# Kernel optimization log

Measured on AMD Instinct MI355X. Metric: run time of the kernel, lower is better.

Reference implementation:

```python
import jax, jax.numpy as jnp
import numpy as np

N_HEAD = 16


def setup_inputs() -> dict:
    key = jax.random.key(0)
    ks = jax.random.split(key, 9)
    B, T, C = 4, 2048, 1024
    s = 1.0 / np.sqrt(C)
    x = jax.random.normal(ks[0], (B, T, C), dtype=jnp.float32)
    Wq = jax.random.normal(ks[1], (C, C), dtype=jnp.float32) * s
    bq = jnp.zeros((C,), dtype=jnp.float32)
    Wk = jax.random.normal(ks[2], (C, C), dtype=jnp.float32) * s
    bk = jnp.zeros((C,), dtype=jnp.float32)
    Wv = jax.random.normal(ks[3], (C, C), dtype=jnp.float32) * s
    bv = jnp.zeros((C,), dtype=jnp.float32)
    Wp = jax.random.normal(ks[4], (C, C), dtype=jnp.float32) * s
    bp = jnp.zeros((C,), dtype=jnp.float32)
    return {"x": x, "Wq": Wq, "bq": bq, "Wk": Wk, "bk": bk,
            "Wv": Wv, "bv": bv, "Wp": Wp, "bp": bp}


def reference(x, Wq, bq, Wk, bk, Wv, bv, Wp, bp):
    B, T, C = x.shape
    H = N_HEAD
    D = C // H
    # QKV projections, then split heads: [B, T, C] -> [B, H, T, D]
    def split_heads(t):
        return t.reshape(B, T, H, D).transpose(0, 2, 1, 3)
    q = split_heads(x @ Wq.T + bq)
    k = split_heads(x @ Wk.T + bk)
    v = split_heads(x @ Wv.T + bv)
    # NOTE: original code applies NO causal mask despite the class name.
    att = jnp.einsum('bhtd,bhsd->bhts', q, k) * (1.0 / jnp.sqrt(jnp.float32(D)))
    att = jax.nn.softmax(att, axis=-1)
    y = jnp.einsum('bhts,bhsd->bhtd', att, v)  # [B, H, T, D]
    y = y.transpose(0, 2, 1, 3).reshape(B, T, C)
    return y @ Wp.T + bp
```

## Files before the change

### kernel.cpp

```cpp
#include <hip/hip_runtime.h>
#include <hip/hip_bf16.h>

typedef float  f32x4   __attribute__((ext_vector_type(4)));
typedef short  bf16x8  __attribute__((ext_vector_type(8)));

__device__ __forceinline__ ushort f2b(float f) {
  union { float f; unsigned u; } x; x.f = f;
  unsigned r = x.u + 0x7fffu + ((x.u >> 16) & 1u);
  return (ushort)(r >> 16);
}

__device__ __forceinline__ unsigned pk2(float lo, float hi) {
  __hip_bfloat162 t = __float22bfloat162_rn(make_float2(lo, hi));
  union { __hip_bfloat162 b; unsigned u; } c; c.b = t; return c.u;
}

__device__ __forceinline__ f32x4 fzero() {
  f32x4 z; z[0] = 0.f; z[1] = 0.f; z[2] = 0.f; z[3] = 0.f; return z;
}

__device__ __forceinline__ void gld_lds16(const ushort* g, ushort* l) {
  __builtin_amdgcn_global_load_lds(g, l, 16, 0, 0);
}

__device__ __forceinline__ int vperm_s(int j64) {
  return (j64 & 0x23) | ((j64 & 0x0C) << 1) | ((j64 & 0x10) >> 2);
}

__global__ __launch_bounds__(256) void f2bf_kernel(const float* __restrict__ in,
                                                   ushort* __restrict__ out, int n4) {
  int idx = blockIdx.x * 256 + threadIdx.x;
  int stride = gridDim.x * 256;
  for (int i = idx; i < n4; i += stride) {
    float4 v = reinterpret_cast<const float4*>(in)[i];
    ushort4 o;
    o.x = f2b(v.x); o.y = f2b(v.y); o.z = f2b(v.z); o.w = f2b(v.w);
    reinterpret_cast<ushort4*>(out)[i] = o;
  }
}

__global__ __launch_bounds__(256) void f2bf_w4(
    const float* __restrict__ w0, const float* __restrict__ w1,
    const float* __restrict__ w2, const float* __restrict__ w3,
    ushort* __restrict__ out, int n4) {
  const float* src = (blockIdx.y == 0) ? w0 : (blockIdx.y == 1) ? w1
                   : (blockIdx.y == 2) ? w2 : w3;
  ushort* dst = out + (size_t)blockIdx.y * (size_t)n4 * 4;
  int idx = blockIdx.x * 256 + threadIdx.x;
  int stride = gridDim.x * 256;
  for (int i = idx; i < n4; i += stride) {
    float4 v = reinterpret_cast<const float4*>(src)[i];
    ushort4 o;
    o.x = f2b(v.x); o.y = f2b(v.y); o.z = f2b(v.z); o.w = f2b(v.w);
    reinterpret_cast<ushort4*>(dst)[i] = o;
  }
}

__global__ __launch_bounds__(256) void gemm_bt_n64(
    const ushort* __restrict__ A, const ushort* __restrict__ B,
    const float* __restrict__ bias, float* __restrict__ Cf,
    int M, int N, int K) {
  __shared__ ushort As[128 * 32];
  __shared__ ushort Bs[64 * 32];
  const int tid = threadIdx.x, lane = tid & 63, wave = tid >> 6;
  const int wr = (wave >> 1) << 6, wc = (wave & 1) << 5;
  const int fr = lane & 15, fk8 = (lane >> 4) << 3;

  const size_t rowA = (size_t)blockIdx.y * 128;
  const size_t rowB = (size_t)blockIdx.x * 64;
  const ushort* Ag = A + rowA * K;
  const ushort* Bg = B + rowB * K;

  const int c0 = tid, c1 = tid + 256;
  const size_t a0 = (size_t)(c0 >> 2) * K + (size_t)((c0 & 3) << 3);
  const size_t a1 = (size_t)(c1 >> 2) * K + (size_t)((c1 & 3) << 3);

  f32x4 acc[4][2];
#pragma unroll
  for (int m = 0; m < 4; ++m)
#pragma unroll
    for (int n = 0; n < 2; ++n) acc[m][n] = fzero();

  for (int k0 = 0; k0 < K; k0 += 32) {
    __syncthreads();
    gld_lds16(Ag + a0 + k0, &As[wave * 512]);
    gld_lds16(Ag + a1 + k0, &As[2048 + wave * 512]);
    gld_lds16(Bg + a0 + k0, &Bs[wave * 512]);
    asm volatile("s_waitcnt vmcnt(0)" ::: "memory");
    __syncthreads();

    bf16x8 af[4], bfv[2];
#pragma unroll
    for (int m = 0; m < 4; ++m)
      af[m] = *reinterpret_cast<const bf16x8*>(&As[(wr + m * 16 + fr) * 32 + fk8]);
#pragma unroll
    for (int n = 0; n < 2; ++n)
      bfv[n] = *reinterpret_cast<const bf16x8*>(&Bs[(wc + n * 16 + fr) * 32 + fk8]);
#pragma unroll
    for (int m = 0; m < 4; ++m)
#pragma unroll
      for (int n = 0; n < 2; ++n)
        acc[m][n] = __builtin_amdgcn_mfma_f32_16x16x32_bf16(af[m], bfv[n], acc[m][n], 0, 0, 0);
  }

  const int orow = (lane >> 4) << 2;
#pragma unroll
  for (int m = 0; m < 4; ++m) {
#pragma unroll
    for (int n = 0; n < 2; ++n) {
      size_t gc = rowB + wc + n * 16 + fr;
      float bv = bias[gc];
#pragma unroll
      for (int r = 0; r < 4; ++r) {
        size_t gr = rowA + wr + m * 16 + orow + r;
        Cf[gr * N + gc] = acc[m][n][r] + bv;
      }
    }
  }
}

__global__ __launch_bounds__(256) void gemm_qkv(
    const ushort* __restrict__ A, const ushort* __restrict__ Bw,
    const float* __restrict__ bq, const float* __restrict__ bk, const float* __restrict__ bv,
    ushort* __restrict__ Qb, ushort* __restrict__ Kb, ushort* __restrict__ VbT,
    float qscale) {
  __shared__ ushort As[128 * 32];
  __shared__ ushort Bs[128 * 32];
  const int tid = threadIdx.x, lane = tid & 63, wave = tid >> 6;
  const int wr = (wave >> 1) << 6, wc = (wave & 1) << 6;
  const int fr = lane & 15, fk8 = (lane >> 4) << 3;
  const int K = 1024;

  const size_t rowA = (size_t)blockIdx.y * 128;
  const size_t rowB = (size_t)blockIdx.x * 128;
  const ushort* Ag = A + rowA * K;
  const ushort* Bg = Bw + rowB * K;

  const int c0 = tid, c1 = tid + 256;
  const size_t a0 = (size_t)(c0 >> 2) * K + (size_t)((c0 & 3) << 3);
  const size_t a1 = (size_t)(c1 >> 2) * K + (size_t)((c1 & 3) << 3);

  f32x4 acc[4][4];
#pragma unroll
  for (int m = 0; m < 4; ++m)
#pragma unroll
    for (int n = 0; n < 4; ++n) acc[m][n] = fzero();

  for (int k0 = 0; k0 < K; k0 += 32) {
    __syncthreads();
    gld_lds16(Ag + a0 + k0, &As[wave * 512]);
    gld_lds16(Ag + a1 + k0, &As[2048 + wave * 512]);
    gld_lds16(Bg + a0 + k0, &Bs[wave * 512]);
    gld_lds16(Bg + a1 + k0, &Bs[2048 + wave * 512]);
    asm volatile("s_waitcnt vmcnt(0)" ::: "memory");
    __syncthreads();

    bf16x8 af[4], bfv[4];
#pragma unroll
    for (int m = 0; m < 4; ++m)
      af[m] = *reinterpret_cast<const bf16x8*>(&As[(wr + m * 16 + fr) * 32 + fk8]);
#pragma unroll
    for (int n = 0; n < 4; ++n)
      bfv[n] = *reinterpret_cast<const bf16x8*>(&Bs[(wc + n * 16 + fr) * 32 + fk8]);
#pragma unroll
    for (int m = 0; m < 4; ++m)
#pragma unroll
      for (int n = 0; n < 4; ++n)
        acc[m][n] = __builtin_amdgcn_mfma_f32_16x16x32_bf16(af[m], bfv[n], acc[m][n], 0, 0, 0);
  }

  const int stripe  = blockIdx.x >> 3;
  const int colbase = (blockIdx.x & 7) * 128;
  const int orow = (lane >> 4) << 2;
#pragma unroll
  for (int m = 0; m < 4; ++m) {
#pragma unroll
    for (int n = 0; n < 4; ++n) {
      const int gcl = colbase + wc + n * 16 + fr;
      if (stripe == 0) {
        const float bb_ = bq[gcl];
#pragma unroll
        for (int r = 0; r < 4; ++r) {
          size_t gr = rowA + wr + m * 16 + orow + r;
          Qb[gr * 1024 + gcl] = f2b((acc[m][n][r] + bb_) * qscale);
        }
      } else if (stripe == 1) {
        const float bb_ = bk[gcl];
#pragma unroll
        for (int r = 0; r < 4; ++r) {
          size_t gr = rowA + wr + m * 16 + orow + r;
          Kb[gr * 1024 + gcl] = f2b(acc[m][n][r] + bb_);
        }
      } else {
        const float bb_ = bv[gcl];
        int tt0 = (int)rowA + wr + m * 16 + orow;
        int b = tt0 >> 11, t = tt0 & 2047;
        size_t idx0 = (size_t)b * 2097152 + (size_t)gcl * 2048
                    + (size_t)((t & ~63) + vperm_s(t & 63));
        ushort4 o;
        o.x = f2b(acc[m][n][0] + bb_);
        o.y = f2b(acc[m][n][1] + bb_);
        o.z = f2b(acc[m][n][2] + bb_);
        o.w = f2b(acc[m][n][3] + bb_);
        *reinterpret_cast<ushort4*>(&VbT[idx0]) = o;
      }
    }
  }
}

__global__ __launch_bounds__(512, 4) void attn_kernel(
    const ushort* __restrict__ Qb, const ushort* __restrict__ Kb,
    const ushort* __restrict__ VbT, ushort* __restrict__ Yb) {
  __shared__ ushort lds[16384];
  const int tid = threadIdx.x, lane = tid & 63, wave = tid >> 6;
  const int fr = lane & 15, g = lane >> 4, fk8 = g << 3;
  const int bb = blockIdx.y >> 4, hh = blockIdx.y & 15;
  const size_t rowbase = (size_t)bb * 2048;
  const int cbase = hh * 64;
  const ushort* Kg  = Kb  + rowbase * 1024 + cbase;
  const ushort* VgT = VbT + (size_t)bb * 2097152 + (size_t)cbase * 2048;

  const int qrow = blockIdx.x * 128 + wave * 16 + fr;
  const ushort* qptr = &Qb[(rowbase + qrow) * 1024 + cbase];
  const bf16x8 qf0 = *reinterpret_cast<const bf16x8*>(qptr + fk8);
  const bf16x8 qf1 = *reinterpret_cast<const bf16x8*>(qptr + 32 + fk8);

  const int rS = tid >> 3;
  const int wS = (tid & 7) ^ (rS & 7);
  const ushort* sKp = Kg  + (size_t)rS * 1024 + (wS << 3);
  const ushort* sVp = VgT + (size_t)rS * 2048 + (wS << 3);
  const int wofs = wave * 512;

  const int e0 = (g ^ (fr & 7)) << 3;
  const int e1 = ((4 + g) ^ (fr & 7)) << 3;
  const ushort* lpA = &lds[fr * 64 + e0];
  const ushort* lpB = &lds[fr * 64 + e1];

  f32x4 yacc[4];
#pragma unroll
  for (int nb = 0; nb < 4; ++nb) yacc[nb] = fzero();
  f32x4 psum4 = fzero();

#define LD8(P) (*reinterpret_cast<const bf16x8*>(P))
#define MF16(A, B, C) __builtin_amdgcn_mfma_f32_16x16x32_bf16(A, B, C, 0, 0, 0)

  gld_lds16(sKp, &lds[wofs]);  gld_lds16(sVp, &lds[8192 + wofs]);  sKp += 65536; sVp += 64;
  asm volatile("s_waitcnt vmcnt(0)" ::: "memory");
  __builtin_amdgcn_s_barrier();
  __builtin_amdgcn_sched_barrier(0);

#define TILE(BUF, DOPF) do {                                                     \
    if (DOPF) {    \
      gld_lds16(sKp, &lds[((BUF) ^ 1) * 4096 + wofs]);                           \
      gld_lds16(sVp, &lds[8192 + ((BUF) ^ 1) * 4096 + wofs]);                    \
      sKp += 65536; sVp += 64;                                                   \
    }                                                                            \
    f32x4 sT[4];                                                                 \
    _Pragma("unroll")                                                            \
    for (int jb = 0; jb < 4; ++jb) {                                             \
      bf16x8 kf0 = LD8(lpA + (BUF) * 4096 + jb * 1024);                          \
      bf16x8 kf1 = LD8(lpB + (BUF) * 4096 + jb * 1024);                          \
      f32x4 z = fzero();                                                         \
      __builtin_amdgcn_s_setprio(1);                                             \
      z = MF16(kf0, qf0, z);                                                     \
      z = MF16(kf1, qf1, z);                                                     \
      __builtin_amdgcn_s_setprio(0);                                             \
      sT[jb] = z;                                                                \
    }                                                                            \
    _Pragma("unroll")                                                            \
    for (int jb = 0; jb < 4; ++jb)                                               \
      _Pragma("unroll")                                                          \
      for (int r = 0; r < 4; ++r) sT[jb][r] = __builtin_exp2f(sT[jb][r]);        \
    _Pragma("unroll")                                                            \
    for (int r = 0; r < 4; ++r)                                                  \
      psum4[r] += (sT[0][r] + sT[1][r]) + (sT[2][r] + sT[3][r]);                 \
    union { bf16x8 v; unsigned u[4]; } pa0, pa1;                                 \
    pa0.u[0] = pk2(sT[0][0], sT[0][1]); pa0.u[1] = pk2(sT[0][2], sT[0][3]);      \
    pa0.u[2] = pk2(sT[1][0], sT[1][1]); pa0.u[3] = pk2(sT[1][2], sT[1][3]);      \
    pa1.u[0] = pk2(sT[2][0], sT[2][1]); pa1.u[1] = pk2(sT[2][2], sT[2][3]);      \
    pa1.u[2] = pk2(sT[3][0], sT[3][1]); pa1.u[3] = pk2(sT[3][2], sT[3][3]);      \
    _Pragma("unroll")                                                            \
    for (int nb = 0; nb < 4; ++nb) {                                             \
      bf16x8 vf0 = LD8(lpA + 8192 + (BUF) * 4096 + nb * 1024);                   \
      bf16x8 vf1 = LD8(lpB + 8192 + (BUF) * 4096 + nb * 1024);                   \
      __builtin_amdgcn_s_setprio(1);                                             \
      yacc[nb] = MF16(vf0, pa0.v, yacc[nb]);                                     \
      yacc[nb] = MF16(vf1, pa1.v, yacc[nb]);                                     \
      __builtin_amdgcn_s_setprio(0);                                             \
    }                                                                            \
    asm volatile("s_waitcnt vmcnt(0)" ::: "memory");                             \
    __builtin_amdgcn_s_barrier();                                                \
    __builtin_amdgcn_sched_barrier(0);                                           \
  } while (0)

  for (int tb = 0; tb < 30; tb += 2) {
    TILE(0, 1);
    TILE(1, 1);
  }
  TILE(0, 1);
  TILE(1, 0);
#undef TILE
#undef MF16
#undef LD8

  float psum = (psum4[0] + psum4[1]) + (psum4[2] + psum4[3]);
  psum += __shfl_xor(psum, 16);
  psum += __shfl_xor(psum, 32);
  const float linv = 1.0f / psum;
  ushort* yrow = &Yb[(rowbase + qrow) * 1024 + cbase];
#pragma unroll
  for (int nb = 0; nb < 4; ++nb) {
    ushort4 o;
    o.x = f2b(yacc[nb][0] * linv);
    o.y = f2b(yacc[nb][1] * linv);
    o.z = f2b(yacc[nb][2] * linv);
    o.w = f2b(yacc[nb][3] * linv);
    *reinterpret_cast<ushort4*>(yrow + nb * 16 + (g << 2)) = o;
  }
}

extern "C" void kernel_launch(void* const* d_in, const int* in_sizes, int n_in,
                              void* d_out, int out_size, void* d_ws, size_t ws_size,
                              hipStream_t stream) {
  const float* x  = (const float*)d_in[0];
  const float* Wq = (const float*)d_in[1];
  const float* bq = (const float*)d_in[2];
  const float* Wk = (const float*)d_in[3];
  const float* bk = (const float*)d_in[4];
  const float* Wv = (const float*)d_in[5];
  const float* bv = (const float*)d_in[6];
  const float* Wp = (const float*)d_in[7];
  const float* bp = (const float*)d_in[8];
  float* out = (float*)d_out;

  const int M = 8192, C = 1024;
  const size_t MC = (size_t)M * C, CC = (size_t)C * C;
  const size_t need = (MC * 5 + CC * 4) * sizeof(ushort);
  if (ws_size < need) return;

  ushort* xb  = (ushort*)d_ws;
  ushort* wqb = xb + MC;
  ushort* wpb = wqb + 3 * CC;
  ushort* Qb  = wpb + CC;
  ushort* Kb  = Qb + MC;
  ushort* VbT = Kb + MC;
  ushort* Yb  = VbT + MC;

  f2bf_kernel<<<2048, 256, 0, stream>>>(x, xb, (int)(MC / 4));
  f2bf_w4<<<dim3(256, 4), 256, 0, stream>>>(Wq, Wk, Wv, Wp, wqb, (int)(CC / 4));

  const float QSCALE = 0.18033688011112042f;
  gemm_qkv<<<dim3(24, 64), 256, 0, stream>>>(xb, wqb, bq, bk, bv, Qb, Kb, VbT, QSCALE);

  attn_kernel<<<dim3(16, 64), 512, 0, stream>>>(Qb, Kb, VbT, Yb);

  gemm_bt_n64<<<dim3(16, 64), 256, 0, stream>>>(Yb, wpb, bp, out, M, C, C);
}
```

Measured before the change: 236.5 us.

## Switch attention to 32x32x16 MFMA with 4-wave blocks and swizzle GEMM grids

The attention kernel moves from 16x16x32 to 32x32x16 bf16 MFMA tiles. Each of 4 waves now owns 32 query rows, so blocks drop to 256 threads and each thread stages two K and two V chunks per tile. The V transpose permutation in the QKV GEMM changes to match the new operand layout. Both GEMMs also remap block indices with an XCD-style swizzle to improve L2 locality. The larger MFMA shape cuts LDS operand reads per FLOP, at the cost of more registers per thread and a different occupancy profile.

```diff
diff --git a/kernel.cpp b/kernel.cpp
--- a/kernel.cpp
+++ b/kernel.cpp
@@ -2,6 +2,7 @@
 #include <hip/hip_bf16.h>
 
 typedef float  f32x4   __attribute__((ext_vector_type(4)));
+typedef float  f32x16  __attribute__((ext_vector_type(16)));
 typedef short  bf16x8  __attribute__((ext_vector_type(8)));
 
 __device__ __forceinline__ ushort f2b(float f) {
@@ -19,12 +20,19 @@
   f32x4 z; z[0] = 0.f; z[1] = 0.f; z[2] = 0.f; z[3] = 0.f; return z;
 }
 
+__device__ __forceinline__ f32x16 fz16() {
+  f32x16 z;
+#pragma unroll
+  for (int i = 0; i < 16; ++i) z[i] = 0.f;
+  return z;
+}
+
 __device__ __forceinline__ void gld_lds16(const ushort* g, ushort* l) {
   __builtin_amdgcn_global_load_lds(g, l, 16, 0, 0);
 }
 
-__device__ __forceinline__ int vperm_s(int j64) {
-  return (j64 & 0x23) | ((j64 & 0x0C) << 1) | ((j64 & 0x10) >> 2);
+__device__ __forceinline__ int vperm16(int j) {
+  return (j & 3) | ((j & 4) << 1) | ((j & 8) >> 1);
 }
 
 __global__ __launch_bounds__(256) void f2bf_kernel(const float* __restrict__ in,
@@ -66,8 +74,12 @@
   const int wr = (wave >> 1) << 6, wc = (wave & 1) << 5;
   const int fr = lane & 15, fk8 = (lane >> 4) << 3;
 
-  const size_t rowA = (size_t)blockIdx.y * 128;
-  const size_t rowB = (size_t)blockIdx.x * 64;
+  const int orig = blockIdx.y * 16 + blockIdx.x;
+  const int swz  = (orig & 7) * 128 + (orig >> 3);
+  const int bx = swz & 15, by = swz >> 4;
+
+  const size_t rowA = (size_t)by * 128;
+  const size_t rowB = (size_t)bx * 64;
   const ushort* Ag = A + rowA * K;
   const ushort* Bg = B + rowB * K;
 
@@ -131,8 +143,12 @@
   const int fr = lane & 15, fk8 = (lane >> 4) << 3;
   const int K = 1024;
 
-  const size_t rowA = (size_t)blockIdx.y * 128;
-  const size_t rowB = (size_t)blockIdx.x * 128;
+  const int orig = blockIdx.y * 24 + blockIdx.x;
+  const int swz  = (orig & 7) * 192 + (orig >> 3);
+  const int bx = swz % 24, by = swz / 24;
+
+  const size_t rowA = (size_t)by * 128;
+  const size_t rowB = (size_t)bx * 128;
   const ushort* Ag = A + rowA * K;
   const ushort* Bg = Bw + rowB * K;
 
@@ -169,8 +185,8 @@
         acc[m][n] = __builtin_amdgcn_mfma_f32_16x16x32_bf16(af[m], bfv[n], acc[m][n], 0, 0, 0);
   }
 
-  const int stripe  = blockIdx.x >> 3;
-  const int colbase = (blockIdx.x & 7) * 128;
+  const int stripe  = bx >> 3;
+  const int colbase = (bx & 7) * 128;
   const int orow = (lane >> 4) << 2;
 #pragma unroll
   for (int m = 0; m < 4; ++m) {
@@ -196,7 +212,7 @@
         int tt0 = (int)rowA + wr + m * 16 + orow;
         int b = tt0 >> 11, t = tt0 & 2047;
         size_t idx0 = (size_t)b * 2097152 + (size_t)gcl * 2048
-                    + (size_t)((t & ~63) + vperm_s(t & 63));
+                    + (size_t)((t & ~15) | vperm16(t & 15));
         ushort4 o;
         o.x = f2b(acc[m][n][0] + bb_);
         o.y = f2b(acc[m][n][1] + bb_);
@@ -208,84 +224,104 @@
   }
 }
 
-__global__ __launch_bounds__(512, 4) void attn_kernel(
+__global__ __launch_bounds__(256, 4) void attn_kernel(
     const ushort* __restrict__ Qb, const ushort* __restrict__ Kb,
     const ushort* __restrict__ VbT, ushort* __restrict__ Yb) {
   __shared__ ushort lds[16384];
   const int tid = threadIdx.x, lane = tid & 63, wave = tid >> 6;
-  const int fr = lane & 15, g = lane >> 4, fk8 = g << 3;
+  const int l31 = lane & 31, h = lane >> 5;
+  const int c0s = h ^ (l31 & 7);
   const int bb = blockIdx.y >> 4, hh = blockIdx.y & 15;
   const size_t rowbase = (size_t)bb * 2048;
   const int cbase = hh * 64;
   const ushort* Kg  = Kb  + rowbase * 1024 + cbase;
   const ushort* VgT = VbT + (size_t)bb * 2097152 + (size_t)cbase * 2048;
 
-  const int qrow = blockIdx.x * 128 + wave * 16 + fr;
-  const ushort* qptr = &Qb[(rowbase + qrow) * 1024 + cbase];
-  const bf16x8 qf0 = *reinterpret_cast<const bf16x8*>(qptr + fk8);
-  const bf16x8 qf1 = *reinterpret_cast<const bf16x8*>(qptr + 32 + fk8);
-
-  const int rS = tid >> 3;
-  const int wS = (tid & 7) ^ (rS & 7);
-  const ushort* sKp = Kg  + (size_t)rS * 1024 + (wS << 3);
-  const ushort* sVp = VgT + (size_t)rS * 2048 + (wS << 3);
+  const int qrow = blockIdx.x * 128 + wave * 32 + l31;
+  const ushort* qptr = &Qb[(rowbase + qrow) * 1024 + cbase + h * 8];
+  const bf16x8 qf0 = *reinterpret_cast<const bf16x8*>(qptr);
+  const bf16x8 qf1 = *reinterpret_cast<const bf16x8*>(qptr + 16);
+  const bf16x8 qf2 = *reinterpret_cast<const bf16x8*>(qptr + 32);
+  const bf16x8 qf3 = *reinterpret_cast<const bf16x8*>(qptr + 48);
+
+  const int r0 = tid >> 3;
+  const int w0 = (tid & 7) ^ (r0 & 7);
+  const ushort* sK0 = Kg  + (size_t)r0 * 1024 + (w0 << 3);
+  const ushort* sK1 = Kg  + (size_t)(r0 + 32) * 1024 + (w0 << 3);
+  const ushort* sV0 = VgT + (size_t)r0 * 2048 + (w0 << 3);
+  const ushort* sV1 = VgT + (size_t)(r0 + 32) * 2048 + (w0 << 3);
   const int wofs = wave * 512;
 
-  const int e0 = (g ^ (fr & 7)) << 3;
-  const int e1 = ((4 + g) ^ (fr & 7)) << 3;
-  const ushort* lpA = &lds[fr * 64 + e0];
-  const ushort* lpB = &lds[fr * 64 + e1];
-
-  f32x4 yacc[4];
-#pragma unroll
-  for (int nb = 0; nb < 4; ++nb) yacc[nb] = fzero();
+  const ushort* lp0 = &lds[l31 * 64 + ((0 ^ c0s) << 3)];
+  const ushort* lp1 = &lds[l31 * 64 + ((2 ^ c0s) << 3)];
+  const ushort* lp2 = &lds[l31 * 64 + ((4 ^ c0s) << 3)];
+  const ushort* lp3 = &lds[l31 * 64 + ((6 ^ c0s) << 3)];
+
+  f32x16 y0 = fz16(), y1 = fz16();
   f32x4 psum4 = fzero();
 
 #define LD8(P) (*reinterpret_cast<const bf16x8*>(P))
-#define MF16(A, B, C) __builtin_amdgcn_mfma_f32_16x16x32_bf16(A, B, C, 0, 0, 0)
-
-  gld_lds16(sKp, &lds[wofs]);  gld_lds16(sVp, &lds[8192 + wofs]);  sKp += 65536; sVp += 64;
+#define MF32(A, B, C) __builtin_amdgcn_mfma_f32_32x32x16_bf16(A, B, C, 0, 0, 0)
+#define STAGE(BUF) do {                                                          \
+    gld_lds16(sK0, &lds[(BUF) * 4096 + wofs]);                                   \
+    gld_lds16(sK1, &lds[(BUF) * 4096 + 2048 + wofs]);                            \
+    gld_lds16(sV0, &lds[8192 + (BUF) * 4096 + wofs]);                            \
+    gld_lds16(sV1, &lds[8192 + (BUF) * 4096 + 2048 + wofs]);                     \
+    sK0 += 65536; sK1 += 65536; sV0 += 64; sV1 += 64;                            \
+  } while (0)
+
+  STAGE(0);
   asm volatile("s_waitcnt vmcnt(0)" ::: "memory");
   __builtin_amdgcn_s_barrier();
   __builtin_amdgcn_sched_barrier(0);
 
+#define QK_BLK(ST, BUF, JB) do {                                                 \
+    bf16x8 k0_ = LD8(lp0 + (BUF) * 4096 + (JB) * 2048);                          \
+    bf16x8 k1_ = LD8(lp1 + (BUF) * 4096 + (JB) * 2048);                          \
+    bf16x8 k2_ = LD8(lp2 + (BUF) * 4096 + (JB) * 2048);                          \
+    bf16x8 k3_ = LD8(lp3 + (BUF) * 4096 + (JB) * 2048);                          \
+    __builtin_amdgcn_s_setprio(1);                                               \
+    ST = MF32(k0_, qf0, ST); ST = MF32(k1_, qf1, ST);                            \
+    ST = MF32(k2_, qf2, ST); ST = MF32(k3_, qf3, ST);                            \
+    __builtin_amdgcn_s_setprio(0);                                               \
+  } while (0)
+
+#define SM_BLK(ST, PA, PB_) do {                                                 \
+    _Pragma("unroll")                                                            \
+    for (int e_ = 0; e_ < 16; ++e_) ST[e_] = __builtin_exp2f(ST[e_]);            \
+    _Pragma("unroll")                                                            \
+    for (int e_ = 0; e_ < 4; ++e_)                                               \
+      psum4[e_] += (ST[e_] + ST[4 + e_]) + (ST[8 + e_] + ST[12 + e_]);           \
+    PA.u[0]  = pk2(ST[0], ST[1]);   PA.u[1]  = pk2(ST[2], ST[3]);                \
+    PA.u[2]  = pk2(ST[4], ST[5]);   PA.u[3]  = pk2(ST[6], ST[7]);                \
+    PB_.u[0] = pk2(ST[8], ST[9]);   PB_.u[1] = pk2(ST[10], ST[11]);              \
+    PB_.u[2] = pk2(ST[12], ST[13]); PB_.u[3] = pk2(ST[14], ST[15]);              \
+  } while (0)
+
 #define TILE(BUF, DOPF) do {                                                     \
-    if (DOPF) {    \
-      gld_lds16(sKp, &lds[((BUF) ^ 1) * 4096 + wofs]);                           \
-      gld_lds16(sVp, &lds[8192 + ((BUF) ^ 1) * 4096 + wofs]);                    \
-      sKp += 65536; sVp += 64;                                                   \
+    if (DOPF) STAGE((BUF) ^ 1);                                                  \
+    union { bf16x8 v; unsigned u[4]; } pa0, pa1, pa2, pa3;                       \
+    {                                                                            \
+      f32x16 st = fz16();                                                        \
+      QK_BLK(st, BUF, 0);                                                        \
+      SM_BLK(st, pa0, pa1);                                                      \
     }                                                                            \
-    f32x4 sT[4];                                                                 \
-    _Pragma("unroll")                                                            \
-    for (int jb = 0; jb < 4; ++jb) {                                             \
-      bf16x8 kf0 = LD8(lpA + (BUF) * 4096 + jb * 1024);                          \
-      bf16x8 kf1 = LD8(lpB + (BUF) * 4096 + jb * 1024);                          \
-      f32x4 z = fzero();                                                         \
+    {                                                                            \
+      f32x16 st = fz16();                                                        \
+      QK_BLK(st, BUF, 1);                                                        \
+      SM_BLK(st, pa2, pa3);                                                      \
+    }                                                                            \
+    {                                                                            \
+      bf16x8 v_;                                                                 \
       __builtin_amdgcn_s_setprio(1);                                             \
-      z = MF16(kf0, qf0, z);                                                     \
-      z = MF16(kf1, qf1, z);                                                     \
-      __builtin_amdgcn_s_setprio(0);                                             \
-      sT[jb] = z;                                                                \
-    }                                                                            \
-    _Pragma("unroll")                                                            \
-    for (int jb = 0; jb < 4; ++jb)                                               \
-      _Pragma("unroll")                                                          \
-      for (int r = 0; r < 4; ++r) sT[jb][r] = __builtin_exp2f(sT[jb][r]);        \
-    _Pragma("unroll")                                                            \
-    for (int r = 0; r < 4; ++r)                                                  \
-      psum4[r] += (sT[0][r] + sT[1][r]) + (sT[2][r] + sT[3][r]);                 \
-    union { bf16x8 v; unsigned u[4]; } pa0, pa1;                                 \
-    pa0.u[0] = pk2(sT[0][0], sT[0][1]); pa0.u[1] = pk2(sT[0][2], sT[0][3]);      \
-    pa0.u[2] = pk2(sT[1][0], sT[1][1]); pa0.u[3] = pk2(sT[1][2], sT[1][3]);      \
-    pa1.u[0] = pk2(sT[2][0], sT[2][1]); pa1.u[1] = pk2(sT[2][2], sT[2][3]);      \
-    pa1.u[2] = pk2(sT[3][0], sT[3][1]); pa1.u[3] = pk2(sT[3][2], sT[3][3]);      \
-    _Pragma("unroll")                                                            \
-    for (int nb = 0; nb < 4; ++nb) {                                             \
-      bf16x8 vf0 = LD8(lpA + 8192 + (BUF) * 4096 + nb * 1024);                   \
-      bf16x8 vf1 = LD8(lpB + 8192 + (BUF) * 4096 + nb * 1024);                   \
-      __builtin_amdgcn_s_setprio(1);                                             \
-      yacc[nb] = MF16(vf0, pa0.v, yacc[nb]);                                     \
-      yacc[nb] = MF16(vf1, pa1.v, yacc[nb]);                                     \
+      v_ = LD8(lp0 + 8192 + (BUF) * 4096);         y0 = MF32(v_, pa0.v, y0);     \
+      v_ = LD8(lp1 + 8192 + (BUF) * 4096);         y0 = MF32(v_, pa1.v, y0);     \
+      v_ = LD8(lp2 + 8192 + (BUF) * 4096);         y0 = MF32(v_, pa2.v, y0);     \
+      v_ = LD8(lp3 + 8192 + (BUF) * 4096);         y0 = MF32(v_, pa3.v, y0);     \
+      v_ = LD8(lp0 + 10240 + (BUF) * 4096);        y1 = MF32(v_, pa0.v, y1);     \
+      v_ = LD8(lp1 + 10240 + (BUF) * 4096);        y1 = MF32(v_, pa1.v, y1);     \
+      v_ = LD8(lp2 + 10240 + (BUF) * 4096);        y1 = MF32(v_, pa2.v, y1);     \
+      v_ = LD8(lp3 + 10240 + (BUF) * 4096);        y1 = MF32(v_, pa3.v, y1);     \
       __builtin_amdgcn_s_setprio(0);                                             \
     }                                                                            \
     asm volatile("s_waitcnt vmcnt(0)" ::: "memory");                             \
@@ -300,22 +336,28 @@
   TILE(0, 1);
   TILE(1, 0);
 #undef TILE
-#undef MF16
+#undef SM_BLK
+#undef QK_BLK
+#undef STAGE
+#undef MF32
 #undef LD8
 
   float psum = (psum4[0] + psum4[1]) + (psum4[2] + psum4[3]);
-  psum += __shfl_xor(psum, 16);
-  psum += __shfl_xor(psum, 32);
-  const float linv = 1.0f / psum;
+  const float ltot = psum + __shfl_xor(psum, 32);
+  const float linv = 1.0f / ltot;
   ushort* yrow = &Yb[(rowbase + qrow) * 1024 + cbase];
 #pragma unroll
-  for (int nb = 0; nb < 4; ++nb) {
-    ushort4 o;
-    o.x = f2b(yacc[nb][0] * linv);
-    o.y = f2b(yacc[nb][1] * linv);
-    o.z = f2b(yacc[nb][2] * linv);
-    o.w = f2b(yacc[nb][3] * linv);
-    *reinterpret_cast<ushort4*>(yrow + nb * 16 + (g << 2)) = o;
+  for (int dblk = 0; dblk < 2; ++dblk) {
+    const f32x16& yy = dblk ? y1 : y0;
+#pragma unroll
+    for (int rq = 0; rq < 4; ++rq) {
+      ushort4 o;
+      o.x = f2b(yy[rq * 4 + 0] * linv);
+      o.y = f2b(yy[rq * 4 + 1] * linv);
+      o.z = f2b(yy[rq * 4 + 2] * linv);
+      o.w = f2b(yy[rq * 4 + 3] * linv);
+      *reinterpret_cast<ushort4*>(yrow + dblk * 32 + rq * 8 + h * 4) = o;
+    }
   }
 }
 
@@ -352,7 +394,7 @@
   const float QSCALE = 0.18033688011112042f;
   gemm_qkv<<<dim3(24, 64), 256, 0, stream>>>(xb, wqb, bq, bk, bv, Qb, Kb, VbT, QSCALE);
 
-  attn_kernel<<<dim3(16, 64), 512, 0, stream>>>(Qb, Kb, VbT, Yb);
+  attn_kernel<<<dim3(16, 64), 256, 0, stream>>>(Qb, Kb, VbT, Yb);
 
   gemm_bt_n64<<<dim3(16, 64), 256, 0, stream>>>(Yb, wpb, bp, out, M, C, C);
 }
```

After: 495.9 us. +109.7%, slower.
